# Kernel optimization log

Hardware: AMD Instinct MI355X
Metric: run time of the kernel (lower is better)

## Reference

```python
import jax, jax.numpy as jnp
import numpy as np

B, H, HKV, S, D = 1, 16, 4, 2048, 128


def setup_inputs() -> dict:
    key = jax.random.key(0)
    kq, kk, kv = jax.random.split(key, 3)
    Q = jax.random.normal(kq, (B, H, S, D), dtype=jnp.float32)
    K = jax.random.normal(kk, (B, HKV, S, D), dtype=jnp.float32)
    V = jax.random.normal(kv, (B, HKV, S, D), dtype=jnp.float32)
    return {"Q": Q, "K": K, "V": V, "causal": 1, "gqa_group_size": 4}


def reference(Q, K, V, causal, gqa_group_size):
    b, h, s, d = Q.shape
    scale = 1.0 / (d ** 0.5)
    if gqa_group_size > 1:
        # repeat_interleave along head dim: [B,Hkv,S,D] -> [B,H,S,D]
        K = jnp.repeat(K, gqa_group_size, axis=1)
        V = jnp.repeat(V, gqa_group_size, axis=1)
    # scores: [B,H,S,S]
    P = jnp.einsum('bhqd,bhkd->bhqk', Q, K) * scale
    if causal:
        mask = jnp.tril(jnp.ones((s, s), dtype=bool))
        P = jnp.where(mask, P, -jnp.inf)
    P = jax.nn.softmax(P.astype(jnp.float32), axis=-1).astype(Q.dtype)
    O = jnp.einsum('bhqk,bhkd->bhqd', P, V)
    return O
```

## Files before the change

kernel.cpp:

```cpp
#include <hip/hip_runtime.h>
#include <hip/hip_bf16.h>


#define NH    16
#define NHKV  4
#define SEQ   2048
#define DIM   128
#define QBLK  64
#define KVBLK 64
#define NT    (SEQ / KVBLK)

typedef __attribute__((ext_vector_type(8)))  short bf16x8_t;
typedef __attribute__((ext_vector_type(16))) float f32x16_t;

__device__ inline ushort f2bf(float f) {
    uint x = __float_as_uint(f);
    uint r = (x + 0x7fffu + ((x >> 16) & 1u)) >> 16;
    return (ushort)r;
}

__device__ inline uint cvtpk_bf16(float lo, float hi) {
    uint r;
    asm("v_cvt_pk_bf16_f32 %0, %1, %2" : "=v"(r) : "v"(lo), "v"(hi));
    return r;
}

#define GLOAD_LDS16(gsrc, ldst) \
    __builtin_amdgcn_global_load_lds( \
        (const __attribute__((address_space(1))) void*)(gsrc), \
        (__attribute__((address_space(3))) void*)(ldst), 16, 0, 0)

extern "C" __global__ __launch_bounds__(256)
void prep_kv(const float* __restrict__ K, const float* __restrict__ V,
             ushort* __restrict__ Kpre, ushort* __restrict__ Vpre)
{
    int gid = blockIdx.x * 256 + threadIdx.x;
    if (blockIdx.x < 1024) {
        int kvh = gid >> 16; int rem = gid & 65535;
        int s = rem >> 5; int dq = (rem & 31) << 2;
        float4 f = *(const float4*)(K + ((size_t)(kvh * SEQ + s)) * DIM + dq);
        uint lo = (uint)f2bf(f.x) | ((uint)f2bf(f.y) << 16);
        uint hi = (uint)f2bf(f.z) | ((uint)f2bf(f.w) << 16);
        int tile = s >> 6, row = s & 63;
        uint byte = ((uint)(row * 256 + dq * 2)) ^ ((uint)(row & 7) << 4);
        *(uint2*)((char*)Kpre + (((size_t)(kvh * NT + tile)) << 14) + byte) =
            make_uint2(lo, hi);
    } else {
        int g2 = gid - 1024 * 256;
        int kvh = g2 >> 16; int rem = g2 & 65535;
        int d = rem & 127; int t2 = rem >> 7;
        int tile = t2 >> 4; int kv = (t2 & 15) << 2;
        const float* b = V + ((size_t)(kvh * SEQ + tile * 64 + kv)) * DIM + d;
        uint lo = (uint)f2bf(b[0])       | ((uint)f2bf(b[DIM]) << 16);
        uint hi = (uint)f2bf(b[2 * DIM]) | ((uint)f2bf(b[3 * DIM]) << 16);
        uint byte = ((uint)(d * 128 + kv * 2)) ^ ((uint)(d & 7) << 4);
        *(uint2*)((char*)Vpre + (((size_t)(kvh * NT + tile)) << 14) + byte) =
            make_uint2(lo, hi);
    }
}

extern "C" __global__ __launch_bounds__(256, 2)
void attn_fwd(const float* __restrict__ Q, const ushort* __restrict__ Kpre,
              const ushort* __restrict__ Vpre, float* __restrict__ O)
{
    const int bid = blockIdx.x;
    const int h   = bid & 15;
    const int p   = bid >> 4;
    const int qt  = (p < 16) ? p : 47 - p;
    const int kvh = h >> 2;
    const int q0  = qt * QBLK;
    const int tid  = threadIdx.x;
    const int w    = tid >> 6;
    const int qh   = w >> 1;
    const int kh   = w & 1;
    const int lane = tid & 63;
    const int q31  = lane & 31;
    const int hi   = lane >> 5;

    __shared__ char smem[65536];
    char* smb = &smem[0];

    const float qscale = 0.08838834764831845f * 1.4426950408889634f;

    bf16x8_t qf[8];
    const int qrow = q0 + qh * 32 + q31;
    {
        const float* qp = Q + ((size_t)h * SEQ + qrow) * DIM + hi * 8;
#pragma unroll
        for (int ks = 0; ks < 8; ++ks) {
            float4 f0 = *(const float4*)(qp + ks * 16);
            float4 f1 = *(const float4*)(qp + ks * 16 + 4);
            bf16x8_t a;
            a[0] = (short)f2bf(f0.x * qscale); a[1] = (short)f2bf(f0.y * qscale);
            a[2] = (short)f2bf(f0.z * qscale); a[3] = (short)f2bf(f0.w * qscale);
            a[4] = (short)f2bf(f1.x * qscale); a[5] = (short)f2bf(f1.y * qscale);
            a[6] = (short)f2bf(f1.z * qscale); a[7] = (short)f2bf(f1.w * qscale);
            qf[ks] = a;
        }
    }

    f32x16_t oacc[4];
#pragma unroll
    for (int m = 0; m < 4; ++m)
#pragma unroll
        for (int i = 0; i < 16; ++i) oacc[m][i] = 0.f;
    float m_r = -1e30f, l_r = 0.f;

    const size_t kvbase = (size_t)kvh * NT;
    const int nt = qt + 1;

    auto stage = [&](int b, int t) {
        const char* kg = (const char*)Kpre + ((kvbase + t) << 14) + tid * 16;
        const char* vg = (const char*)Vpre + ((kvbase + t) << 14) + tid * 16;
        char* kl = smb + b * 16384 + tid * 16;
        char* vl = smb + 32768 + b * 16384 + tid * 16;
#pragma unroll
        for (int c = 0; c < 4; ++c) {
            GLOAD_LDS16(kg + c * 4096, kl + c * 4096);
            GLOAD_LDS16(vg + c * 4096, vl + c * 4096);
        }
    };

    stage(0, 0);
    __syncthreads();
    int buf = 0;

    const int  kvrow = kh * 32 + q31;
    const uint kswz  = ((uint)(kvrow & 7)) << 4;

    for (int t = 0; t < nt; ++t) {
        if (t + 1 < nt) stage(buf ^ 1, t + 1);
        const bool diag = (t == nt - 1);

        if (!(diag && w == 1)) {
            f32x16_t sacc;
#pragma unroll
            for (int i = 0; i < 16; ++i) sacc[i] = 0.f;
            const char* kb = smb + buf * 16384;
            __builtin_amdgcn_s_setprio(1);
#pragma unroll
            for (int ks = 0; ks < 8; ++ks) {
                uint byte = ((uint)(kvrow * 256 + ks * 32 + hi * 16)) ^ kswz;
                bf16x8_t kf = *(bf16x8_t*)(kb + byte);
                sacc = __builtin_amdgcn_mfma_f32_32x32x16_bf16(kf, qf[ks], sacc, 0, 0, 0);
            }
            __builtin_amdgcn_s_setprio(0);

            if (diag && (w == 0 || w == 3)) {
#pragma unroll
                for (int reg = 0; reg < 16; ++reg) {
                    int crow = (reg & 3) + 8 * (reg >> 2) + 4 * hi;
                    if (crow > q31) sacc[reg] = -1e30f;
                }
            }

            float pmax = sacc[0];
#pragma unroll
            for (int i = 1; i < 16; ++i) pmax = fmaxf(pmax, sacc[i]);
            pmax = fmaxf(pmax, __shfl_xor(pmax, 32, 64));

            if (!__all(pmax - m_r <= 8.f)) {
                float mnew = fmaxf(m_r, pmax);
                float alpha = __builtin_exp2f(m_r - mnew);
                m_r = mnew;
                l_r *= alpha;
#pragma unroll
                for (int m = 0; m < 4; ++m)
#pragma unroll
                    for (int i = 0; i < 16; ++i) oacc[m][i] *= alpha;
            }

            float pv[16];
            float psum = 0.f;
#pragma unroll
            for (int i = 0; i < 16; ++i) {
                pv[i] = __builtin_exp2f(sacc[i] - m_r);
                psum += pv[i];
            }
            psum += __shfl_xor(psum, 32, 64);
            l_r += psum;

            bf16x8_t pa[2];
#pragma unroll
            for (int hf = 0; hf < 2; ++hf) {
                uint a0 = cvtpk_bf16(pv[hf * 8 + 0], pv[hf * 8 + 1]);
                uint a1 = cvtpk_bf16(pv[hf * 8 + 2], pv[hf * 8 + 3]);
                uint b0 = cvtpk_bf16(pv[hf * 8 + 4], pv[hf * 8 + 5]);
                uint b1 = cvtpk_bf16(pv[hf * 8 + 6], pv[hf * 8 + 7]);
                asm volatile("v_permlane32_swap_b32 %0, %1" : "+v"(a0), "+v"(b0));
                asm volatile("v_permlane32_swap_b32 %0, %1" : "+v"(a1), "+v"(b1));
                uint4 tmp = make_uint4(a0, a1, b0, b1);
                pa[hf] = *(bf16x8_t*)&tmp;
            }

            const char* vb = smb + 32768 + buf * 16384;
            __builtin_amdgcn_s_setprio(1);
#pragma unroll
            for (int m = 0; m < 4; ++m) {
                const int drow = m * 32 + q31;
                const uint vswz = ((uint)(drow & 7)) << 4;
#pragma unroll
                for (int ks2 = 0; ks2 < 2; ++ks2) {
                    uint byte = ((uint)(drow * 128 + kh * 64 + ks2 * 32 + hi * 16)) ^ vswz;
                    bf16x8_t vf = *(bf16x8_t*)(vb + byte);
                    oacc[m] = __builtin_amdgcn_mfma_f32_32x32x16_bf16(vf, pa[ks2], oacc[m], 0, 0, 0);
                }
            }
            __builtin_amdgcn_s_setprio(0);
        }

        __syncthreads();
        buf ^= 1;
    }

    float* fb  = (float*)smb;
    float* fb2 = fb + 128;
    if (kh == 1) {
        if (hi == 0) { fb[qh * 64 + q31] = m_r; fb[qh * 64 + 32 + q31] = l_r; }
#pragma unroll
        for (int m = 0; m < 4; ++m)
#pragma unroll
            for (int reg = 0; reg < 16; ++reg) {
                int d = m * 32 + (reg & 3) + 8 * (reg >> 2) + 4 * hi;
                fb2[(qh * 128 + d) * 32 + q31] = oacc[m][reg];
            }
    }
    __syncthreads();
    if (kh == 0) {
        float m1 = fb[qh * 64 + q31];
        float l1 = fb[qh * 64 + 32 + q31];
        float mN = fmaxf(m_r, m1);
        float a0 = __builtin_exp2f(m_r - mN);
        float a1 = __builtin_exp2f(m1 - mN);
        float inv = 1.0f / (l_r * a0 + l1 * a1);
        a0 *= inv; a1 *= inv;
        float* op = O + ((size_t)h * SEQ + qrow) * DIM;
#pragma unroll
        for (int m = 0; m < 4; ++m)
#pragma unroll
            for (int rq = 0; rq < 4; ++rq) {
                int d0 = m * 32 + 8 * rq + 4 * hi;
                float4 v;
                v.x = oacc[m][rq * 4 + 0] * a0 + fb2[(qh * 128 + d0 + 0) * 32 + q31] * a1;
                v.y = oacc[m][rq * 4 + 1] * a0 + fb2[(qh * 128 + d0 + 1) * 32 + q31] * a1;
                v.z = oacc[m][rq * 4 + 2] * a0 + fb2[(qh * 128 + d0 + 2) * 32 + q31] * a1;
                v.w = oacc[m][rq * 4 + 3] * a0 + fb2[(qh * 128 + d0 + 3) * 32 + q31] * a1;
                *(float4*)(op + d0) = v;
            }
    }
}

extern "C" void kernel_launch(void* const* d_in, const int* in_sizes, int n_in,
                              void* d_out, int out_size, void* d_ws, size_t ws_size,
                              hipStream_t stream) {
    const float* Q = (const float*)d_in[0];
    const float* K = (const float*)d_in[1];
    const float* V = (const float*)d_in[2];
    float* O = (float*)d_out;
    ushort* Kpre = (ushort*)d_ws;
    ushort* Vpre = (ushort*)((char*)d_ws + (2u << 20));
    prep_kv<<<2048, 256, 0, stream>>>(K, V, Kpre, Vpre);
    attn_fwd<<<dim3(512), 256, 0, stream>>>(Q, Kpre, Vpre, O);
}
```

Before: 120.9 us.

## Split K/V staging into triple-buffered K and double-buffered V with vmcnt waits

Staging of K and V tiles is split into separate async loads, with K triple-buffered two tiles ahead and V double-buffered one tile ahead. Each iteration now has two barriers gated by explicit s_waitcnt vmcnt counts, so the QK^T phase waits only for K and the PV phase only for V. The goal is more overlap of global-to-LDS traffic with MFMA work. The cost is LDS growing from 64KB to 80KB, which with launch bounds of 2 blocks per CU may reduce occupancy, and the hand-counted vmcnt values are fragile.

```diff
diff --git a/kernel.cpp b/kernel.cpp
--- a/kernel.cpp
+++ b/kernel.cpp
@@ -29,6 +29,8 @@
     __builtin_amdgcn_global_load_lds( \
         (const __attribute__((address_space(1))) void*)(gsrc), \
         (__attribute__((address_space(3))) void*)(ldst), 16, 0, 0)
+
+#define WAITV(n) asm volatile("s_waitcnt vmcnt(" #n ")" ::: "memory")
 
 extern "C" __global__ __launch_bounds__(256)
 void prep_kv(const float* __restrict__ K, const float* __restrict__ V,
@@ -77,7 +79,7 @@
     const int q31  = lane & 31;
     const int hi   = lane >> 5;
 
-    __shared__ char smem[65536];
+    __shared__ char smem[81920];
     char* smb = &smem[0];
 
     const float qscale = 0.08838834764831845f * 1.4426950408889634f;
@@ -109,34 +111,46 @@
     const size_t kvbase = (size_t)kvh * NT;
     const int nt = qt + 1;
 
-    auto stage = [&](int b, int t) {
+    auto stageK = [&](int slot, int t) {
         const char* kg = (const char*)Kpre + ((kvbase + t) << 14) + tid * 16;
+        char* kl = smb + slot * 16384 + tid * 16;
+#pragma unroll
+        for (int c = 0; c < 4; ++c) GLOAD_LDS16(kg + c * 4096, kl + c * 4096);
+    };
+    auto stageV = [&](int slot, int t) {
         const char* vg = (const char*)Vpre + ((kvbase + t) << 14) + tid * 16;
-        char* kl = smb + b * 16384 + tid * 16;
-        char* vl = smb + 32768 + b * 16384 + tid * 16;
-#pragma unroll
-        for (int c = 0; c < 4; ++c) {
-            GLOAD_LDS16(kg + c * 4096, kl + c * 4096);
-            GLOAD_LDS16(vg + c * 4096, vl + c * 4096);
-        }
+        char* vl = smb + 49152 + slot * 16384 + tid * 16;
+#pragma unroll
+        for (int c = 0; c < 4; ++c) GLOAD_LDS16(vg + c * 4096, vl + c * 4096);
     };
 
-    stage(0, 0);
-    __syncthreads();
-    int buf = 0;
+    stageK(0, 0);
+    if (nt >= 2) stageK(1, 1);
+    stageV(0, 0);
 
     const int  kvrow = kh * 32 + q31;
     const uint kswz  = ((uint)(kvrow & 7)) << 4;
 
+    int kcur = 0;
+
     for (int t = 0; t < nt; ++t) {
-        if (t + 1 < nt) stage(buf ^ 1, t + 1);
         const bool diag = (t == nt - 1);
-
-        if (!(diag && w == 1)) {
-            f32x16_t sacc;
+        const bool active = !(diag && w == 1);
+
+        if (t == nt - 1) { WAITV(4); } else { WAITV(8); }
+        __builtin_amdgcn_s_barrier();
+        __builtin_amdgcn_sched_barrier(0);
+
+        if (t + 1 < nt) stageV((t + 1) & 1, t + 1);
+        if (t + 2 < nt) { int k2 = kcur + 2 >= 3 ? kcur - 1 : kcur + 2; stageK(k2, t + 2); }
+
+        f32x16_t sacc;
+        float pv[16];
+        bf16x8_t pa[2];
+        if (active) {
 #pragma unroll
             for (int i = 0; i < 16; ++i) sacc[i] = 0.f;
-            const char* kb = smb + buf * 16384;
+            const char* kb = smb + kcur * 16384;
             __builtin_amdgcn_s_setprio(1);
 #pragma unroll
             for (int ks = 0; ks < 8; ++ks) {
@@ -170,7 +184,6 @@
                     for (int i = 0; i < 16; ++i) oacc[m][i] *= alpha;
             }
 
-            float pv[16];
             float psum = 0.f;
 #pragma unroll
             for (int i = 0; i < 16; ++i) {
@@ -180,7 +193,6 @@
             psum += __shfl_xor(psum, 32, 64);
             l_r += psum;
 
-            bf16x8_t pa[2];
 #pragma unroll
             for (int hf = 0; hf < 2; ++hf) {
                 uint a0 = cvtpk_bf16(pv[hf * 8 + 0], pv[hf * 8 + 1]);
@@ -192,8 +204,18 @@
                 uint4 tmp = make_uint4(a0, a1, b0, b1);
                 pa[hf] = *(bf16x8_t*)&tmp;
             }
-
-            const char* vb = smb + 32768 + buf * 16384;
+        }
+
+        if (t == 0) {
+            if (nt >= 3) { WAITV(8); } else if (nt == 2) { WAITV(4); } else { WAITV(0); }
+        } else {
+            if (t + 2 < nt) { WAITV(12); } else if (t + 1 < nt) { WAITV(8); } else { WAITV(0); }
+        }
+        __builtin_amdgcn_s_barrier();
+        __builtin_amdgcn_sched_barrier(0);
+
+        if (active) {
+            const char* vb = smb + 49152 + (t & 1) * 16384;
             __builtin_amdgcn_s_setprio(1);
 #pragma unroll
             for (int m = 0; m < 4; ++m) {
@@ -209,10 +231,10 @@
             __builtin_amdgcn_s_setprio(0);
         }
 
-        __syncthreads();
-        buf ^= 1;
-    }
-
+        kcur = (kcur + 1 == 3) ? 0 : kcur + 1;
+    }
+
+    __syncthreads();
     float* fb  = (float*)smb;
     float* fb2 = fb + 128;
     if (kh == 1) {
```

After: 125.5 us. +3.8%, slower.

## Split KV tile across four waves with 128-row tiles and tree reduction

Applied to the files above, without the earlier changes.

Doubles the KV tile to 128 rows and the block to 512 threads, so each of two q-halves is processed by four waves that each own a 32-row KV slice. The causal diagonal is handled by a per-wave offset check, which skips fully masked slices and masks only the diagonal one. The partial softmax states are merged through shared memory with a two-step tree reduction. Double buffering is dropped in favour of a single buffer with syncs around each load, which exposes load latency. It also adds a heavier epilogue reduction and more barriers.

```diff
diff --git a/kernel.cpp b/kernel.cpp
--- a/kernel.cpp
+++ b/kernel.cpp
@@ -7,8 +7,8 @@
 #define SEQ   2048
 #define DIM   128
 #define QBLK  64
-#define KVBLK 64
-#define NT    (SEQ / KVBLK)
+#define KVBLK 128
+#define NT128 (SEQ / KVBLK)
 
 typedef __attribute__((ext_vector_type(8)))  short bf16x8_t;
 typedef __attribute__((ext_vector_type(16))) float f32x16_t;
@@ -41,25 +41,25 @@
         float4 f = *(const float4*)(K + ((size_t)(kvh * SEQ + s)) * DIM + dq);
         uint lo = (uint)f2bf(f.x) | ((uint)f2bf(f.y) << 16);
         uint hi = (uint)f2bf(f.z) | ((uint)f2bf(f.w) << 16);
-        int tile = s >> 6, row = s & 63;
+        int tile = s >> 7, row = s & 127;
         uint byte = ((uint)(row * 256 + dq * 2)) ^ ((uint)(row & 7) << 4);
-        *(uint2*)((char*)Kpre + (((size_t)(kvh * NT + tile)) << 14) + byte) =
+        *(uint2*)((char*)Kpre + (((size_t)(kvh * NT128 + tile)) << 15) + byte) =
             make_uint2(lo, hi);
     } else {
         int g2 = gid - 1024 * 256;
         int kvh = g2 >> 16; int rem = g2 & 65535;
         int d = rem & 127; int t2 = rem >> 7;
-        int tile = t2 >> 4; int kv = (t2 & 15) << 2;
-        const float* b = V + ((size_t)(kvh * SEQ + tile * 64 + kv)) * DIM + d;
+        int tile = t2 >> 5; int kvq = (t2 & 31) << 2;
+        const float* b = V + ((size_t)(kvh * SEQ + tile * KVBLK + kvq)) * DIM + d;
         uint lo = (uint)f2bf(b[0])       | ((uint)f2bf(b[DIM]) << 16);
         uint hi = (uint)f2bf(b[2 * DIM]) | ((uint)f2bf(b[3 * DIM]) << 16);
-        uint byte = ((uint)(d * 128 + kv * 2)) ^ ((uint)(d & 7) << 4);
-        *(uint2*)((char*)Vpre + (((size_t)(kvh * NT + tile)) << 14) + byte) =
+        uint byte = ((uint)(d * 256 + kvq * 2)) ^ ((uint)(d & 7) << 4);
+        *(uint2*)((char*)Vpre + (((size_t)(kvh * NT128 + tile)) << 15) + byte) =
             make_uint2(lo, hi);
     }
 }
 
-extern "C" __global__ __launch_bounds__(256, 2)
+extern "C" __global__ __launch_bounds__(512, 4)
 void attn_fwd(const float* __restrict__ Q, const ushort* __restrict__ Kpre,
               const ushort* __restrict__ Vpre, float* __restrict__ O)
 {
@@ -71,8 +71,8 @@
     const int q0  = qt * QBLK;
     const int tid  = threadIdx.x;
     const int w    = tid >> 6;
-    const int qh   = w >> 1;
-    const int kh   = w & 1;
+    const int qh   = w >> 2;
+    const int kq   = w & 3;
     const int lane = tid & 63;
     const int q31  = lane & 31;
     const int hi   = lane >> 5;
@@ -106,47 +106,43 @@
         for (int i = 0; i < 16; ++i) oacc[m][i] = 0.f;
     float m_r = -1e30f, l_r = 0.f;
 
-    const size_t kvbase = (size_t)kvh * NT;
-    const int nt = qt + 1;
-
-    auto stage = [&](int b, int t) {
-        const char* kg = (const char*)Kpre + ((kvbase + t) << 14) + tid * 16;
-        const char* vg = (const char*)Vpre + ((kvbase + t) << 14) + tid * 16;
-        char* kl = smb + b * 16384 + tid * 16;
-        char* vl = smb + 32768 + b * 16384 + tid * 16;
-#pragma unroll
-        for (int c = 0; c < 4; ++c) {
-            GLOAD_LDS16(kg + c * 4096, kl + c * 4096);
-            GLOAD_LDS16(vg + c * 4096, vl + c * 4096);
-        }
-    };
-
-    stage(0, 0);
-    __syncthreads();
-    int buf = 0;
-
-    const int  kvrow = kh * 32 + q31;
-    const uint kswz  = ((uint)(kvrow & 7)) << 4;
+    const int nt = (qt >> 1) + 1;
+    const size_t kvbase = (size_t)kvh * NT128;
+
+    const int  krow = kq * 32 + q31;
+    const uint kswz = ((uint)(krow & 7)) << 4;
 
     for (int t = 0; t < nt; ++t) {
-        if (t + 1 < nt) stage(buf ^ 1, t + 1);
-        const bool diag = (t == nt - 1);
-
-        if (!(diag && w == 1)) {
+        __syncthreads();
+        {
+            const char* kg = (const char*)Kpre + ((kvbase + t) << 15) + tid * 16;
+            const char* vg = (const char*)Vpre + ((kvbase + t) << 15) + tid * 16;
+            char* kl = smb + tid * 16;
+            char* vl = smb + 32768 + tid * 16;
+#pragma unroll
+            for (int c = 0; c < 4; ++c) {
+                GLOAD_LDS16(kg + c * 8192, kl + c * 8192);
+                GLOAD_LDS16(vg + c * 8192, vl + c * 8192);
+            }
+        }
+        __syncthreads();
+
+        int off = 32;
+        if (t == nt - 1) off = q0 + qh * 32 - (t * KVBLK + kq * 32);
+        if (off >= 0) {
             f32x16_t sacc;
 #pragma unroll
             for (int i = 0; i < 16; ++i) sacc[i] = 0.f;
-            const char* kb = smb + buf * 16384;
             __builtin_amdgcn_s_setprio(1);
 #pragma unroll
             for (int ks = 0; ks < 8; ++ks) {
-                uint byte = ((uint)(kvrow * 256 + ks * 32 + hi * 16)) ^ kswz;
-                bf16x8_t kf = *(bf16x8_t*)(kb + byte);
+                uint byte = ((uint)(krow * 256 + ks * 32 + hi * 16)) ^ kswz;
+                bf16x8_t kf = *(bf16x8_t*)(smb + byte);
                 sacc = __builtin_amdgcn_mfma_f32_32x32x16_bf16(kf, qf[ks], sacc, 0, 0, 0);
             }
             __builtin_amdgcn_s_setprio(0);
 
-            if (diag && (w == 0 || w == 3)) {
+            if (off == 0) {
 #pragma unroll
                 for (int reg = 0; reg < 16; ++reg) {
                     int crow = (reg & 3) + 8 * (reg >> 2) + 4 * hi;
@@ -193,7 +189,7 @@
                 pa[hf] = *(bf16x8_t*)&tmp;
             }
 
-            const char* vb = smb + 32768 + buf * 16384;
+            const char* vb = smb + 32768;
             __builtin_amdgcn_s_setprio(1);
 #pragma unroll
             for (int m = 0; m < 4; ++m) {
@@ -201,52 +197,95 @@
                 const uint vswz = ((uint)(drow & 7)) << 4;
 #pragma unroll
                 for (int ks2 = 0; ks2 < 2; ++ks2) {
-                    uint byte = ((uint)(drow * 128 + kh * 64 + ks2 * 32 + hi * 16)) ^ vswz;
+                    uint byte = ((uint)(drow * 256 + kq * 64 + ks2 * 32 + hi * 16)) ^ vswz;
                     bf16x8_t vf = *(bf16x8_t*)(vb + byte);
                     oacc[m] = __builtin_amdgcn_mfma_f32_32x32x16_bf16(vf, pa[ks2], oacc[m], 0, 0, 0);
                 }
             }
             __builtin_amdgcn_s_setprio(0);
         }
-
-        __syncthreads();
-        buf ^= 1;
-    }
-
-    float* fb  = (float*)smb;
-    float* fb2 = fb + 128;
-    if (kh == 1) {
-        if (hi == 0) { fb[qh * 64 + q31] = m_r; fb[qh * 64 + 32 + q31] = l_r; }
-#pragma unroll
-        for (int m = 0; m < 4; ++m)
-#pragma unroll
-            for (int reg = 0; reg < 16; ++reg) {
-                int d = m * 32 + (reg & 3) + 8 * (reg >> 2) + 4 * hi;
-                fb2[(qh * 128 + d) * 32 + q31] = oacc[m][reg];
-            }
-    }
+    }
+
     __syncthreads();
-    if (kh == 0) {
-        float m1 = fb[qh * 64 + q31];
-        float l1 = fb[qh * 64 + 32 + q31];
-        float mN = fmaxf(m_r, m1);
-        float a0 = __builtin_exp2f(m_r - mN);
-        float a1 = __builtin_exp2f(m1 - mN);
-        float inv = 1.0f / (l_r * a0 + l1 * a1);
-        a0 *= inv; a1 *= inv;
-        float* op = O + ((size_t)h * SEQ + qrow) * DIM;
-#pragma unroll
-        for (int m = 0; m < 4; ++m)
-#pragma unroll
-            for (int rq = 0; rq < 4; ++rq) {
-                int d0 = m * 32 + 8 * rq + 4 * hi;
-                float4 v;
-                v.x = oacc[m][rq * 4 + 0] * a0 + fb2[(qh * 128 + d0 + 0) * 32 + q31] * a1;
-                v.y = oacc[m][rq * 4 + 1] * a0 + fb2[(qh * 128 + d0 + 1) * 32 + q31] * a1;
-                v.z = oacc[m][rq * 4 + 2] * a0 + fb2[(qh * 128 + d0 + 2) * 32 + q31] * a1;
-                v.w = oacc[m][rq * 4 + 3] * a0 + fb2[(qh * 128 + d0 + 3) * 32 + q31] * a1;
-                *(float4*)(op + d0) = v;
-            }
+    float* ml = (float*)smb;
+    if (hi == 0) {
+        ml[((qh * 4 + kq) * 2 + 0) * 32 + q31] = m_r;
+        ml[((qh * 4 + kq) * 2 + 1) * 32 + q31] = l_r;
+    }
+    __syncthreads();
+    float mN = -1e30f;
+#pragma unroll
+    for (int i = 0; i < 4; ++i)
+        mN = fmaxf(mN, ml[((qh * 4 + i) * 2 + 0) * 32 + q31]);
+    float L = 0.f;
+#pragma unroll
+    for (int i = 0; i < 4; ++i)
+        L += __builtin_exp2f(ml[((qh * 4 + i) * 2 + 0) * 32 + q31] - mN)
+             * ml[((qh * 4 + i) * 2 + 1) * 32 + q31];
+    float scale = __builtin_exp2f(m_r - mN) / L;
+#pragma unroll
+    for (int m = 0; m < 4; ++m)
+#pragma unroll
+        for (int i = 0; i < 16; ++i) oacc[m][i] *= scale;
+    __syncthreads();
+
+    float* reg0 = (float*)smb;
+    float* reg1 = (float*)(smb + 32768);
+    {
+        if (kq == 1 || kq == 3) {
+            float* dst = (kq == 1) ? reg0 : reg1;
+#pragma unroll
+            for (int m = 0; m < 4; ++m)
+#pragma unroll
+                for (int g = 0; g < 16; ++g) {
+                    int d = m * 32 + (g & 3) + 8 * (g >> 2) + 4 * hi;
+                    dst[(qh * 128 + d) * 32 + q31] = oacc[m][g];
+                }
+        }
+        __syncthreads();
+        if (kq == 0 || kq == 2) {
+            const float* src = (kq == 0) ? reg0 : reg1;
+#pragma unroll
+            for (int m = 0; m < 4; ++m)
+#pragma unroll
+                for (int g = 0; g < 16; ++g) {
+                    int d = m * 32 + (g & 3) + 8 * (g >> 2) + 4 * hi;
+                    oacc[m][g] += src[(qh * 128 + d) * 32 + q31];
+                }
+        }
+        __syncthreads();
+        if (kq == 2) {
+#pragma unroll
+            for (int m = 0; m < 4; ++m)
+#pragma unroll
+                for (int g = 0; g < 16; ++g) {
+                    int d = m * 32 + (g & 3) + 8 * (g >> 2) + 4 * hi;
+                    reg0[(qh * 128 + d) * 32 + q31] = oacc[m][g];
+                }
+        }
+        __syncthreads();
+        if (kq == 0) {
+#pragma unroll
+            for (int m = 0; m < 4; ++m)
+#pragma unroll
+                for (int g = 0; g < 16; ++g) {
+                    int d = m * 32 + (g & 3) + 8 * (g >> 2) + 4 * hi;
+                    oacc[m][g] += reg0[(qh * 128 + d) * 32 + q31];
+                }
+            float* op = O + ((size_t)h * SEQ + qrow) * DIM;
+#pragma unroll
+            for (int m = 0; m < 4; ++m)
+#pragma unroll
+                for (int rq = 0; rq < 4; ++rq) {
+                    int d0 = m * 32 + 8 * rq + 4 * hi;
+                    float4 v;
+                    v.x = oacc[m][rq * 4 + 0];
+                    v.y = oacc[m][rq * 4 + 1];
+                    v.z = oacc[m][rq * 4 + 2];
+                    v.w = oacc[m][rq * 4 + 3];
+                    *(float4*)(op + d0) = v;
+                }
+        }
     }
 }
 
@@ -260,5 +299,5 @@
     ushort* Kpre = (ushort*)d_ws;
     ushort* Vpre = (ushort*)((char*)d_ws + (2u << 20));
     prep_kv<<<2048, 256, 0, stream>>>(K, V, Kpre, Vpre);
-    attn_fwd<<<dim3(512), 256, 0, stream>>>(Q, Kpre, Vpre, O);
-}
+    attn_fwd<<<dim3(512), 512, 0, stream>>>(Q, Kpre, Vpre, O);
+}
```

New measurement: 144.4 us. +19.4%, slower.
